# Optimization experiments

Measured on AMD Instinct MI355X. Metric: run time of the kernel, lower is better.

## Reference

```python
import jax, jax.numpy as jnp
import numpy as np

IN_DIM, HID, MID, FFN, OUT = 384, 128, 1024, 512, 1024
B, T = 8, 4096
LN_EPS = 1e-5


def _legs_hippo(n: int) -> np.ndarray:
    # A[i, j] = P_i(2j/n - 1) * sqrt(2i + 1), Legendre via 3-term recurrence
    x = 2.0 * np.arange(n) / n - 1.0          # eval points, shape [n]
    P = np.zeros((n, n), dtype=np.float64)     # P[i] = P_i(x)
    P[0] = 1.0
    if n > 1:
        P[1] = x
    for i in range(1, n - 1):
        P[i + 1] = ((2 * i + 1) * x * P[i] - i * P[i - 1]) / (i + 1)
    A = P * np.sqrt(2.0 * np.arange(n) + 1.0)[:, None]
    # rescale so the 4096-step recurrence stays finite (A is a free Parameter,
    # so any test value is valid; unscaled LegS overflows fp32 in ~20 steps)
    s = np.linalg.norm(A, 2)
    return (A / (1.05 * s)).astype(np.float32)


def _layernorm(x, g, b):
    mu = jnp.mean(x, axis=-1, keepdims=True)
    var = jnp.var(x, axis=-1, keepdims=True)
    return (x - mu) * jax.lax.rsqrt(var + LN_EPS) * g + b


def setup_inputs() -> dict:
    key = jax.random.key(0)
    ks = jax.random.split(key, 16)

    def w(k, shape, fan_in):
        return jax.random.normal(k, shape, jnp.float32) * (1.0 / np.sqrt(fan_in))

    return {
        "padded_x": jax.random.normal(ks[0], (B, T, IN_DIM), jnp.float32),
        "seq_lens": jax.random.randint(ks[1], (B,), 1, T + 1, jnp.int32),
        "A": jnp.asarray(_legs_hippo(HID)),
        "enc_w1": w(ks[2], (IN_DIM, MID), IN_DIM), "enc_b1": jnp.zeros((MID,), jnp.float32),
        "enc_w2": w(ks[3], (MID, HID), MID), "enc_b2": jnp.zeros((HID,), jnp.float32),
        "proj_w": w(ks[4], (HID, MID), HID), "proj_b": jnp.zeros((MID,), jnp.float32),
        "ln1_g": jnp.ones((MID,), jnp.float32), "ln1_b": jnp.zeros((MID,), jnp.float32),
        "ffn_w1": w(ks[5], (MID, FFN), MID), "ffn_b1": jnp.zeros((FFN,), jnp.float32),
        "ffn_w2": w(ks[6], (FFN, OUT), FFN), "ffn_b2": jnp.zeros((OUT,), jnp.float32),
        "ln2_g": jnp.ones((OUT,), jnp.float32), "ln2_b": jnp.zeros((OUT,), jnp.float32),
        "out_w": w(ks[7], (OUT, OUT), OUT), "out_b": jnp.zeros((OUT,), jnp.float32),
    }


def reference(padded_x, seq_lens, A, enc_w1, enc_b1, enc_w2, enc_b2,
              proj_w, proj_b, ln1_g, ln1_b, ffn_w1, ffn_b1, ffn_w2, ffn_b2,
              ln2_g, ln2_b, out_w, out_b):
    # encoder: Linear -> GELU(exact) -> Linear   [B, T, HID]
    h_mid = jax.nn.gelu(padded_x @ enc_w1 + enc_b1, approximate=False)
    seqs_bx = h_mid @ enc_w2 + enc_b2

    # masked linear recurrence h_t = A @ h_{t-1} + Bx_t via lax.scan over time
    xs = jnp.swapaxes(seqs_bx, 0, 1)           # [T, B, HID]
    ts = jnp.arange(xs.shape[0])

    def step(h, inp):
        x_t, t = inp
        upd = h @ A.T + x_t                     # (A @ h)^T batched
        mask = (t < seq_lens)[:, None]          # [B, 1]
        return jnp.where(mask, upd, h), None

    h0 = jnp.zeros((padded_x.shape[0], A.shape[0]), padded_x.dtype)
    batch_h, _ = jax.lax.scan(step, h0, (xs, ts))

    # decoder
    projected = batch_h @ proj_w + proj_b
    norm_h = _layernorm(projected, ln1_g, ln1_b)
    ffn_out = jax.nn.gelu(norm_h @ ffn_w1 + ffn_b1, approximate=False) @ ffn_w2 + ffn_b2
    ffn_out = ffn_out + projected               # residual (requires OUT == MID)
    norm_ffn = _layernorm(ffn_out, ln2_g, ln2_b)
    return norm_ffn @ out_w + out_b             # [B, OUT]
```

## Files before the change

### kernel.cpp

```cpp
#include <hip/hip_runtime.h>

typedef __attribute__((ext_vector_type(8))) short short8;
typedef __attribute__((ext_vector_type(4))) short short4v;
typedef __attribute__((ext_vector_type(4))) float float4v;

__device__ __forceinline__ float bf2f(short s) {
  union { float f; unsigned u; } cv; cv.u = ((unsigned)(unsigned short)s) << 16; return cv.f;
}
__device__ __forceinline__ short f2bf(float f) {
  union { float f; unsigned u; } cv; cv.f = f;
  unsigned u = cv.u;
  unsigned r = u + 0x7FFFu + ((u >> 16) & 1u);
  return (short)(r >> 16);
}
__device__ __forceinline__ float gelu_f(float v) {
  return 0.5f * v * (1.0f + erff(v * 0.70710678118654752440f));
}
__device__ __forceinline__ void glds16(const short* g, short* l) {
  __builtin_amdgcn_global_load_lds(
      (const __attribute__((address_space(1))) void*)g,
      (__attribute__((address_space(3))) void*)l, 16, 0, 0);
}

__global__ __launch_bounds__(256) void enc_fused(
    const short* __restrict__ xB, const short* __restrict__ w1T,
    const short* __restrict__ w2T, const float* __restrict__ b1,
    const float* __restrict__ b2, short* __restrict__ seqs,
    const int* __restrict__ seq_lens)
{
  int m0 = blockIdx.x * 64;
  { int b = m0 >> 12, t = m0 & 4095; if (t >= seq_lens[b]) return; }

  __shared__ __align__(16) short As[64 * 64];
  __shared__ __align__(16) short Ws[128 * 64];
  __shared__ __align__(16) short midb[64 * 128];

  int tid = threadIdx.x, lane = tid & 63, wave = tid >> 6;
  int l15 = lane & 15, quad = lane >> 4;
  int lr = lane >> 3, lseg = lane & 7;

  float4v accO[4][2];
#pragma unroll
  for (int i = 0; i < 4; i++)
#pragma unroll
    for (int j = 0; j < 2; j++) accO[i][j] = 0;

  for (int nc = 0; nc < 8; ++nc) {
    float4v accM[4][2];
#pragma unroll
    for (int i = 0; i < 4; i++)
#pragma unroll
      for (int j = 0; j < 2; j++) accM[i][j] = 0;

    for (int ks = 0; ks < 6; ++ks) {
      int kk = ks * 64;
#pragma unroll
      for (int i = 0; i < 2; i++) {
        int rowg = wave * 16 + i * 8;
        glds16(xB + (size_t)(m0 + rowg + lr) * 384 + kk + (lseg ^ lr) * 8, &As[rowg * 64]);
      }
#pragma unroll
      for (int i = 0; i < 4; i++) {
        int rowg = wave * 32 + i * 8;
        glds16(w1T + (size_t)(nc * 128 + rowg + lr) * 384 + kk + (lseg ^ lr) * 8, &Ws[rowg * 64]);
      }
      __syncthreads();
#pragma unroll
      for (int kh = 0; kh < 2; kh++) {
        int s = kh * 4 + quad;
        short8 af[4], bfr[2];
#pragma unroll
        for (int im = 0; im < 4; im++) {
          int r = im * 16 + l15;
          af[im] = *(short8*)&As[r * 64 + ((s ^ (r & 7)) * 8)];
        }
#pragma unroll
        for (int in = 0; in < 2; in++) {
          int r = wave * 32 + in * 16 + l15;
          bfr[in] = *(short8*)&Ws[r * 64 + ((s ^ (r & 7)) * 8)];
        }
#pragma unroll
        for (int im = 0; im < 4; im++)
#pragma unroll
          for (int in = 0; in < 2; in++)
            accM[im][in] = __builtin_amdgcn_mfma_f32_16x16x32_bf16(af[im], bfr[in], accM[im][in], 0, 0, 0);
      }
      __syncthreads();
    }
#pragma unroll
    for (int im = 0; im < 4; im++)
#pragma unroll
      for (int in = 0; in < 2; in++) {
        int k = wave * 32 + in * 16 + l15;
        float bias = b1[nc * 128 + k];
#pragma unroll
        for (int reg = 0; reg < 4; reg++) {
          int m = im * 16 + quad * 4 + reg;
          float v = gelu_f(accM[im][in][reg] + bias);
          int s = k >> 3;
          int sw = (s & 8) | ((s & 7) ^ (m & 7));
          midb[m * 128 + sw * 8 + (k & 7)] = f2bf(v);
        }
      }
    __syncthreads();
#pragma unroll
    for (int ks2 = 0; ks2 < 2; ++ks2) {
      int kk = nc * 128 + ks2 * 64;
#pragma unroll
      for (int i = 0; i < 4; i++) {
        int rowg = wave * 32 + i * 8;
        glds16(w2T + (size_t)(rowg + lr) * 1024 + kk + (lseg ^ lr) * 8, &Ws[rowg * 64]);
      }
      __syncthreads();
#pragma unroll
      for (int kh = 0; kh < 2; kh++) {
        short8 af[4], bfr[2];
#pragma unroll
        for (int im = 0; im < 4; im++) {
          int m = im * 16 + l15;
          int kb = ks2 * 64 + kh * 32 + quad * 8;
          int s = kb >> 3;
          int sw = (s & 8) | ((s & 7) ^ (m & 7));
          af[im] = *(short8*)&midb[m * 128 + sw * 8];
        }
#pragma unroll
        for (int in = 0; in < 2; in++) {
          int r = wave * 32 + in * 16 + l15;
          int s = kh * 4 + quad;
          bfr[in] = *(short8*)&Ws[r * 64 + ((s ^ (r & 7)) * 8)];
        }
#pragma unroll
        for (int im = 0; im < 4; im++)
#pragma unroll
          for (int in = 0; in < 2; in++)
            accO[im][in] = __builtin_amdgcn_mfma_f32_16x16x32_bf16(af[im], bfr[in], accO[im][in], 0, 0, 0);
      }
      __syncthreads();
    }
  }
#pragma unroll
  for (int im = 0; im < 4; im++)
#pragma unroll
    for (int in = 0; in < 2; in++) {
      int n = wave * 32 + in * 16 + l15;
      float bias = b2[n];
#pragma unroll
      for (int reg = 0; reg < 4; reg++) {
        int m = m0 + im * 16 + quad * 4 + reg;
        seqs[(size_t)m * 128 + n] = f2bf(accO[im][in][reg] + bias);
      }
    }
}

__global__ __launch_bounds__(256) void gemm_bt(
    const short* __restrict__ A_, const short* __restrict__ BT,
    float* __restrict__ out, int lda, int ldb, int ldc,
    int kSteps, int kChunk)
{
  int m0 = blockIdx.y * 128;
  int n0 = blockIdx.x * 128;
  int kBase = blockIdx.z * kChunk;

  __shared__ __align__(16) short As[128 * 64];
  __shared__ __align__(16) short Bs[128 * 64];

  int tid = threadIdx.x;
  int lane = tid & 63, wave = tid >> 6;
  int l15 = lane & 15, quad = lane >> 4;
  int wm = wave & 1, wn = wave >> 1;
  int lr = lane >> 3, lseg = lane & 7;

  float4v acc[4][4];
#pragma unroll
  for (int i = 0; i < 4; i++)
#pragma unroll
    for (int j = 0; j < 4; j++) acc[i][j] = 0;

  for (int ks = 0; ks < kSteps; ++ks) {
    int kk = kBase + ks * 64;
#pragma unroll
    for (int i = 0; i < 4; i++) {
      int rowg = wave * 32 + i * 8;
      glds16(A_ + (size_t)(m0 + rowg + lr) * lda + kk + (lseg ^ lr) * 8, &As[rowg * 64]);
      glds16(BT + (size_t)(n0 + rowg + lr) * ldb + kk + (lseg ^ lr) * 8, &Bs[rowg * 64]);
    }
    __syncthreads();
#pragma unroll
    for (int kh = 0; kh < 2; kh++) {
      int s = kh * 4 + quad;
      short8 af[4], bfr[4];
#pragma unroll
      for (int im = 0; im < 4; im++) {
        int r = wm * 64 + im * 16 + l15;
        af[im] = *(short8*)&As[r * 64 + ((s ^ (r & 7)) * 8)];
      }
#pragma unroll
      for (int in = 0; in < 4; in++) {
        int r = wn * 64 + in * 16 + l15;
        bfr[in] = *(short8*)&Bs[r * 64 + ((s ^ (r & 7)) * 8)];
      }
#pragma unroll
      for (int im = 0; im < 4; im++)
#pragma unroll
        for (int in = 0; in < 4; in++)
          acc[im][in] = __builtin_amdgcn_mfma_f32_16x16x32_bf16(af[im], bfr[in], acc[im][in], 0, 0, 0);
    }
    __syncthreads();
  }
  float* outz = out + (size_t)blockIdx.z * 65536;
#pragma unroll
  for (int im = 0; im < 4; im++)
#pragma unroll
    for (int in = 0; in < 4; in++) {
      int n = n0 + wn * 64 + in * 16 + l15;
#pragma unroll
      for (int reg = 0; reg < 4; reg++) {
        int m = m0 + wm * 64 + im * 16 + quad * 4 + reg;
        outz[(size_t)m * ldc + n] = acc[im][in][reg];
      }
    }
}

__global__ void prep_wide(const float* __restrict__ x, const float* __restrict__ w1,
                          const float* __restrict__ w2,
                          const float* __restrict__ proj_w, const float* __restrict__ ffn_w1,
                          const float* __restrict__ ffn_w2, const float* __restrict__ out_w,
                          const float* __restrict__ A,
                          short* __restrict__ xB,
                          short* __restrict__ w1T, short* __restrict__ w2T,
                          short* __restrict__ projB, short* __restrict__ ffn1B,
                          short* __restrict__ ffn2B, short* __restrict__ outB,
                          short* __restrict__ P1, short* __restrict__ P1t,
                          short* __restrict__ P2t,
                          short* __restrict__ Spow, short* __restrict__ SpowT)
{
  int idx = blockIdx.x * 256 + threadIdx.x;
  if (idx < 3145728) {
    float4v v = ((const float4v*)x)[idx];
    short4v o;
#pragma unroll
    for (int j = 0; j < 4; j++) o[j] = f2bf(v[j]);
    ((short4v*)xB)[idx] = o;
    return;
  }
  idx -= 3145728;
  if (idx < 393216) {
    int n = idx / 384, k = idx % 384;
    w1T[idx] = f2bf(w1[k * 1024 + n]);
    return;
  }
  idx -= 393216;
  if (idx < 131072) {
    int n = idx / 1024, k = idx % 1024;
    w2T[idx] = f2bf(w2[k * 128 + n]);
    return;
  }
  idx -= 131072;
  if (idx < 131072) { projB[idx] = f2bf(proj_w[idx]); return; }
  idx -= 131072;
  if (idx < 524288) { ffn1B[idx] = f2bf(ffn_w1[idx]); return; }
  idx -= 524288;
  if (idx < 524288) { ffn2B[idx] = f2bf(ffn_w2[idx]); return; }
  idx -= 524288;
  if (idx < 1048576) { outB[idx] = f2bf(out_w[idx]); return; }
  idx -= 1048576;
  if (idx < 16384) {
    int i = idx >> 7, j = idx & 127;
    short bidv = f2bf((i == j) ? 1.0f : 0.0f);
    P1[i * 8192 + 63 * 128 + j] = bidv;
    P1t[(63 * 128 + j) * 128 + i] = bidv;
    P2t[(63 * 128 + j) * 128 + i] = bidv;
    short ab = f2bf(A[idx]);
    Spow[idx] = ab;
    SpowT[(size_t)j * 128 + i] = ab;
  }
}

__global__ __launch_bounds__(256) void pow_chain(short* __restrict__ Spow,
                                                 short* __restrict__ SpowT)
{
  __shared__ short X[16384];
  __shared__ short XT[16384];
  int t = threadIdx.x;
  for (int i = t * 8; i < 16384; i += 2048) {
    *(short8*)&X[i]  = *(const short8*)&Spow[i];
    *(short8*)&XT[i] = *(const short8*)&SpowT[i];
  }
  __syncthreads();
  int lane = t & 63, wave = t >> 6, l15 = lane & 15, quad = lane >> 4;
  for (int step = 1; step <= 11; ++step) {
    short8 af[2][4], bfr[8][4];
#pragma unroll
    for (int mt = 0; mt < 2; mt++)
#pragma unroll
      for (int ks = 0; ks < 4; ks++)
        af[mt][ks] = *(short8*)&X[(wave * 32 + mt * 16 + l15) * 128 + ks * 32 + quad * 8];
#pragma unroll
    for (int nt = 0; nt < 8; nt++)
#pragma unroll
      for (int ks = 0; ks < 4; ks++)
        bfr[nt][ks] = *(short8*)&XT[(nt * 16 + l15) * 128 + ks * 32 + quad * 8];
    __syncthreads();
    float4v acc[2][8];
#pragma unroll
    for (int mt = 0; mt < 2; mt++)
#pragma unroll
      for (int nt = 0; nt < 8; nt++) acc[mt][nt] = 0;
#pragma unroll
    for (int ks = 0; ks < 4; ks++)
#pragma unroll
      for (int mt = 0; mt < 2; mt++)
#pragma unroll
        for (int nt = 0; nt < 8; nt++)
          acc[mt][nt] = __builtin_amdgcn_mfma_f32_16x16x32_bf16(af[mt][ks], bfr[nt][ks], acc[mt][nt], 0, 0, 0);
    short* gX  = Spow  + (size_t)step * 16384;
    short* gXT = SpowT + (size_t)step * 16384;
#pragma unroll
    for (int mt = 0; mt < 2; mt++)
#pragma unroll
      for (int nt = 0; nt < 8; nt++)
#pragma unroll
        for (int reg = 0; reg < 4; reg++) {
          int m = wave * 32 + mt * 16 + quad * 4 + reg;
          int n = nt * 16 + l15;
          short v = f2bf(acc[mt][nt][reg]);
          X[m * 128 + n] = v; XT[n * 128 + m] = v;
          gX[m * 128 + n] = v; gXT[n * 128 + m] = v;
        }
    __syncthreads();
  }
}

__global__ __launch_bounds__(256) void pow_fill(const short* __restrict__ Spow,
                                                const short* __restrict__ SpowT,
                                                short* __restrict__ P1,
                                                short* __restrict__ P1t,
                                                short* __restrict__ P2t)
{
  __shared__ short cur[16384];
  __shared__ short Bt[16384];
  int bid = blockIdx.x;
  int table1 = bid < 63;
  int e = table1 ? bid + 1 : bid - 62;
  int t = threadIdx.x;
  int lane = t & 63, wave = t >> 6, l15 = lane & 15, quad = lane >> 4;

  int bits = e;
  int k0 = __ffs(bits) - 1; bits &= bits - 1;
  int s0 = table1 ? k0 : (k0 == 0 ? 6 : 6 + k0);
  for (int i = t * 8; i < 16384; i += 2048)
    *(short8*)&cur[i] = *(const short8*)&Spow[(size_t)s0 * 16384 + i];

  while (bits) {
    int k = __ffs(bits) - 1; bits &= bits - 1;
    int si = table1 ? k : (k == 0 ? 6 : 6 + k);
    for (int i = t * 8; i < 16384; i += 2048)
      *(short8*)&Bt[i] = *(const short8*)&SpowT[(size_t)si * 16384 + i];
    __syncthreads();
    short8 af[2][4], bfr[8][4];
#pragma unroll
    for (int mt = 0; mt < 2; mt++)
#pragma unroll
      for (int ks = 0; ks < 4; ks++)
        af[mt][ks] = *(short8*)&cur[(wave * 32 + mt * 16 + l15) * 128 + ks * 32 + quad * 8];
#pragma unroll
    for (int nt = 0; nt < 8; nt++)
#pragma unroll
      for (int ks = 0; ks < 4; ks++)
        bfr[nt][ks] = *(short8*)&Bt[(nt * 16 + l15) * 128 + ks * 32 + quad * 8];
    __syncthreads();
    float4v acc[2][8];
#pragma unroll
    for (int mt = 0; mt < 2; mt++)
#pragma unroll
      for (int nt = 0; nt < 8; nt++) acc[mt][nt] = 0;
#pragma unroll
    for (int ks = 0; ks < 4; ks++)
#pragma unroll
      for (int mt = 0; mt < 2; mt++)
#pragma unroll
        for (int nt = 0; nt < 8; nt++)
          acc[mt][nt] = __builtin_amdgcn_mfma_f32_16x16x32_bf16(af[mt][ks], bfr[nt][ks], acc[mt][nt], 0, 0, 0);
#pragma unroll
    for (int mt = 0; mt < 2; mt++)
#pragma unroll
      for (int nt = 0; nt < 8; nt++)
#pragma unroll
        for (int reg = 0; reg < 4; reg++) {
          int m = wave * 32 + mt * 16 + quad * 4 + reg;
          int n = nt * 16 + l15;
          cur[m * 128 + n] = f2bf(acc[mt][nt][reg]);
        }
    __syncthreads();
  }
  __syncthreads();
  int slot = 63 - e;
  for (int idx = t; idx < 16384; idx += 256) {
    int i = idx >> 7, j = idx & 127;
    short v = cur[idx];
    if (table1) {
      P1[i * 8192 + slot * 128 + j] = v;
      P1t[(slot * 128 + j) * 128 + i] = v;
    } else {
      P2t[(slot * 128 + j) * 128 + i] = v;
    }
  }
}

__global__ __launch_bounds__(256) void combine_gemm(
    const float* __restrict__ Vz, const short* __restrict__ seqs,
    const int* __restrict__ seq_lens,
    const short* __restrict__ P2t, const short* __restrict__ P1t,
    float* __restrict__ hFtail)
{
  __shared__ short X[512 * 8];
  int pp = blockIdx.x >> 4, ks = blockIdx.x & 15;
  int t = threadIdx.x;
  for (int e = t; e < 4096; e += 256) {
    int klocal = e >> 3, b = e & 7;
    int cp = ks * 4 + (klocal >> 7), i = klocal & 127;
    int L = seq_lens[b];
    if (pp == 0) {
      int F = L >> 6, sh = 64 - F;
      float v = 0.f;
      if (cp >= sh) {
        int row = (b * 64 + (cp - sh)) * 128 + i;
#pragma unroll
        for (int z = 0; z < 16; z++) v += Vz[(size_t)z * 65536 + row];
      }
      X[e] = f2bf(v);
    } else {
      int F = L >> 6, rr = L & 63, sh = 64 - rr;
      short s = 0;
      if (cp >= sh) s = seqs[((size_t)b * 4096 + F * 64 + (cp - sh)) * 128 + i];
      X[e] = s;
    }
  }
  __syncthreads();
  const short* P = pp ? P1t : P2t;
  float* outp = hFtail + pp * 1024;
  int i = t & 127, g = t >> 7;
  float acc[4] = {0, 0, 0, 0};
  for (int kl = 0; kl < 512; ++kl) {
    int k = ks * 512 + kl;
    float pv = bf2f(P[k * 128 + i]);
    short4v xv = *(const short4v*)(X + kl * 8 + g * 4);
#pragma unroll
    for (int q = 0; q < 4; q++) acc[q] += bf2f(xv[q]) * pv;
  }
#pragma unroll
  for (int q = 0; q < 4; q++) atomicAdd(&outp[(g * 4 + q) * 128 + i], acc[q]);
}

__global__ __launch_bounds__(256) void proj_stage(
    const float* __restrict__ hFtail, const short* __restrict__ P1t,
    const int* __restrict__ seq_lens, const short* __restrict__ projB,
    const float* __restrict__ proj_b, float* __restrict__ projected)
{
  __shared__ short hT[128 * 8];
  __shared__ float red[4][64][8];
  int t = threadIdx.x;
  {
    int b = t >> 5, i4 = (t & 31) * 4;
    int rr = seq_lens[b] & 63;
    const short* M = P1t + (size_t)(63 - rr) * 128 * 128;
    const float* hF = hFtail + b * 128;
    float acc[4];
#pragma unroll
    for (int q = 0; q < 4; q++) acc[q] = hFtail[1024 + b * 128 + i4 + q];
    for (int j = 0; j < 128; ++j) {
      float hv = hF[j];
      short4v mv = *(const short4v*)&M[j * 128 + i4];
#pragma unroll
      for (int q = 0; q < 4; q++) acc[q] += bf2f(mv[q]) * hv;
    }
#pragma unroll
    for (int q = 0; q < 4; q++) hT[(i4 + q) * 8 + b] = f2bf(acc[q]);
  }
  __syncthreads();
  int c = t & 63, sl = t >> 6;
  int n = blockIdx.x * 64 + c;
  float acc[8] = {0, 0, 0, 0, 0, 0, 0, 0};
  for (int k = sl * 32; k < sl * 32 + 32; ++k) {
    short8 xv = *(short8*)&hT[k * 8];
    float wv = bf2f(projB[k * 1024 + n]);
#pragma unroll
    for (int b = 0; b < 8; b++) acc[b] += bf2f(xv[b]) * wv;
  }
#pragma unroll
  for (int b = 0; b < 8; b++) red[sl][c][b] = acc[b];
  __syncthreads();
  if (sl == 0) {
#pragma unroll
    for (int s = 1; s < 4; s++)
#pragma unroll
      for (int b = 0; b < 8; b++) acc[b] += red[s][c][b];
    float bn = proj_b[n];
#pragma unroll
    for (int b = 0; b < 8; b++) projected[b * 1024 + n] = acc[b] + bn;
  }
}

__global__ __launch_bounds__(256) void ffn1_stage(
    const float* __restrict__ projected, const float* __restrict__ g1,
    const float* __restrict__ b1, const short* __restrict__ ffn1B,
    float* __restrict__ ffn1raw)
{
  __shared__ float part[8][32][2];
  __shared__ float stats[8][2];
  __shared__ short xT[256 * 8];
  __shared__ float red[4][64][8];
  int t = threadIdx.x;
  { int b = t >> 5, j0 = t & 31; float s = 0, q = 0;
    for (int k = j0 * 32; k < j0 * 32 + 32; ++k) { float v = projected[b * 1024 + k]; s += v; q += v * v; }
    part[b][j0][0] = s; part[b][j0][1] = q; }
  __syncthreads();
  if (t < 8) {
    float s = 0, q = 0;
    for (int j = 0; j < 32; j++) { s += part[t][j][0]; q += part[t][j][1]; }
    float mu = s * (1.0f / 1024.0f);
    float var = q * (1.0f / 1024.0f) - mu * mu;
    stats[t][0] = mu; stats[t][1] = rsqrtf(var + 1e-5f);
  }
  __syncthreads();
  int ky0 = blockIdx.y * 256;
  for (int idx = t; idx < 2048; idx += 256) {
    int kl = idx >> 3, b = idx & 7; int k = ky0 + kl;
    float v = (projected[b * 1024 + k] - stats[b][0]) * stats[b][1] * g1[k] + b1[k];
    xT[kl * 8 + b] = f2bf(v);
  }
  __syncthreads();
  int c = t & 63, sl = t >> 6;
  int n = blockIdx.x * 64 + c;
  float acc[8] = {0, 0, 0, 0, 0, 0, 0, 0};
  for (int kl = sl * 64; kl < sl * 64 + 64; ++kl) {
    short8 xv = *(short8*)&xT[kl * 8];
    float wv = bf2f(ffn1B[(size_t)(ky0 + kl) * 512 + n]);
#pragma unroll
    for (int b = 0; b < 8; b++) acc[b] += bf2f(xv[b]) * wv;
  }
#pragma unroll
  for (int b = 0; b < 8; b++) red[sl][c][b] = acc[b];
  __syncthreads();
  if (sl == 0) {
#pragma unroll
    for (int s = 1; s < 4; s++)
#pragma unroll
      for (int b = 0; b < 8; b++) acc[b] += red[s][c][b];
#pragma unroll
    for (int b = 0; b < 8; b++) atomicAdd(&ffn1raw[b * 512 + n], acc[b]);
  }
}

__global__ __launch_bounds__(256) void ffn2_stage(
    const float* __restrict__ ffn1raw, const float* __restrict__ fb1,
    const short* __restrict__ ffn2B, float* __restrict__ ffn2raw)
{
  __shared__ short xT[256 * 8];
  __shared__ float red[4][64][8];
  int t = threadIdx.x;
  int ky0 = blockIdx.y * 256;
  for (int idx = t; idx < 2048; idx += 256) {
    int kl = idx >> 3, b = idx & 7; int k = ky0 + kl;
    float v = gelu_f(ffn1raw[b * 512 + k] + fb1[k]);
    xT[kl * 8 + b] = f2bf(v);
  }
  __syncthreads();
  int c = t & 63, sl = t >> 6;
  int n = blockIdx.x * 64 + c;
  float acc[8] = {0, 0, 0, 0, 0, 0, 0, 0};
  for (int kl = sl * 64; kl < sl * 64 + 64; ++kl) {
    short8 xv = *(short8*)&xT[kl * 8];
    float wv = bf2f(ffn2B[(size_t)(ky0 + kl) * 1024 + n]);
#pragma unroll
    for (int b = 0; b < 8; b++) acc[b] += bf2f(xv[b]) * wv;
  }
#pragma unroll
  for (int b = 0; b < 8; b++) red[sl][c][b] = acc[b];
  __syncthreads();
  if (sl == 0) {
#pragma unroll
    for (int s = 1; s < 4; s++)
#pragma unroll
      for (int b = 0; b < 8; b++) acc[b] += red[s][c][b];
#pragma unroll
    for (int b = 0; b < 8; b++) atomicAdd(&ffn2raw[b * 1024 + n], acc[b]);
  }
}

__global__ __launch_bounds__(256) void out_stage(
    const float* __restrict__ ffn2raw, const float* __restrict__ fb2,
    const float* __restrict__ projected, const float* __restrict__ g2,
    const float* __restrict__ b2ln, const short* __restrict__ outB,
    const float* __restrict__ out_b, float* __restrict__ d_out)
{
  __shared__ float part[8][32][2];
  __shared__ float stats[8][2];
  __shared__ short xT[512 * 8];
  __shared__ float red[4][64][8];
  int t = threadIdx.x;
  { int b = t >> 5, j0 = t & 31; float s = 0, q = 0;
    for (int k = j0 * 32; k < j0 * 32 + 32; ++k) {
      float v = ffn2raw[b * 1024 + k] + fb2[k] + projected[b * 1024 + k];
      s += v; q += v * v;
    }
    part[b][j0][0] = s; part[b][j0][1] = q; }
  __syncthreads();
  if (t < 8) {
    float s = 0, q = 0;
    for (int j = 0; j < 32; j++) { s += part[t][j][0]; q += part[t][j][1]; }
    float mu = s * (1.0f / 1024.0f);
    float var = q * (1.0f / 1024.0f) - mu * mu;
    stats[t][0] = mu; stats[t][1] = rsqrtf(var + 1e-5f);
  }
  __syncthreads();
  int ky0 = blockIdx.y * 512;
  for (int idx = t; idx < 4096; idx += 256) {
    int kl = idx >> 3, b = idx & 7; int k = ky0 + kl;
    float v = ffn2raw[b * 1024 + k] + fb2[k] + projected[b * 1024 + k];
    v = (v - stats[b][0]) * stats[b][1] * g2[k] + b2ln[k];
    xT[kl * 8 + b] = f2bf(v);
  }
  __syncthreads();
  int c = t & 63, sl = t >> 6;
  int n = blockIdx.x * 64 + c;
  float acc[8] = {0, 0, 0, 0, 0, 0, 0, 0};
  for (int kl = sl * 128; kl < sl * 128 + 128; ++kl) {
    short8 xv = *(short8*)&xT[kl * 8];
    float wv = bf2f(outB[(size_t)(ky0 + kl) * 1024 + n]);
#pragma unroll
    for (int b = 0; b < 8; b++) acc[b] += bf2f(xv[b]) * wv;
  }
#pragma unroll
  for (int b = 0; b < 8; b++) red[sl][c][b] = acc[b];
  __syncthreads();
  if (sl == 0) {
#pragma unroll
    for (int s = 1; s < 4; s++)
#pragma unroll
      for (int b = 0; b < 8; b++) acc[b] += red[s][c][b];
    float bn = (blockIdx.y == 0) ? out_b[n] : 0.0f;
#pragma unroll
    for (int b = 0; b < 8; b++) atomicAdd(&d_out[b * 1024 + n], acc[b] + bn);
  }
}

extern "C" void kernel_launch(void* const* d_in, const int* in_sizes, int n_in,
                              void* d_out, int out_size, void* d_ws, size_t ws_size,
                              hipStream_t stream)
{
  (void)in_sizes; (void)n_in; (void)out_size; (void)ws_size;
  const float* x      = (const float*)d_in[0];
  const int* seq_lens = (const int*)d_in[1];
  const float* A      = (const float*)d_in[2];
  const float* enc_w1 = (const float*)d_in[3];
  const float* enc_b1 = (const float*)d_in[4];
  const float* enc_w2 = (const float*)d_in[5];
  const float* enc_b2 = (const float*)d_in[6];
  const float* proj_w = (const float*)d_in[7];
  const float* proj_b = (const float*)d_in[8];
  const float* ln1_g  = (const float*)d_in[9];
  const float* ln1_b  = (const float*)d_in[10];
  const float* ffn_w1 = (const float*)d_in[11];
  const float* ffn_b1 = (const float*)d_in[12];
  const float* ffn_w2 = (const float*)d_in[13];
  const float* ffn_b2 = (const float*)d_in[14];
  const float* ln2_g  = (const float*)d_in[15];
  const float* ln2_b  = (const float*)d_in[16];
  const float* out_w  = (const float*)d_in[17];
  const float* out_b  = (const float*)d_in[18];

  char* p = (char*)d_ws;
  auto alloc = [&](size_t bytes) { char* r = p; p += (bytes + 255) & ~(size_t)255; return r; };
  short* xB    = (short*)alloc(32768ull * 384 * 2);
  short* seqs  = (short*)alloc(32768ull * 128 * 2);
  short* w1T   = (short*)alloc(1024ull * 384 * 2);
  short* w2T   = (short*)alloc(128ull * 1024 * 2);
  short* projB = (short*)alloc(128ull * 1024 * 2);
  short* ffn1B = (short*)alloc(1024ull * 512 * 2);
  short* ffn2B = (short*)alloc(512ull * 1024 * 2);
  short* outB  = (short*)alloc(1024ull * 1024 * 2);
  short* Spow  = (short*)alloc(12ull * 16384 * 2);
  short* SpowT = (short*)alloc(12ull * 16384 * 2);
  short* P1    = (short*)alloc(128ull * 8192 * 2);
  short* P1t   = (short*)alloc(8192ull * 128 * 2);
  short* P2t   = (short*)alloc(8192ull * 128 * 2);
  float* Vz    = (float*)alloc(16ull * 512 * 128 * 4);
  float* hFtail  = (float*)alloc(2ull * 8 * 128 * 4);
  float* ffn1raw = (float*)alloc(8ull * 512 * 4);
  float* ffn2raw = (float*)alloc(8ull * 1024 * 4);
  float* projected = (float*)alloc(8ull * 1024 * 4);

  hipMemsetAsync(hFtail, 0, (2ull * 8 * 128 + 8ull * 512 + 8ull * 1024) * 4, stream);
  hipMemsetAsync(d_out, 0, 8192ull * 4, stream);

  prep_wide<<<23104, 256, 0, stream>>>(x, enc_w1, enc_w2, proj_w, ffn_w1, ffn_w2, out_w, A,
      xB, w1T, w2T, projB, ffn1B, ffn2B, outB, P1, P1t, P2t, Spow, SpowT);
  pow_chain<<<1, 256, 0, stream>>>(Spow, SpowT);
  pow_fill<<<126, 256, 0, stream>>>(Spow, SpowT, P1, P1t, P2t);

  enc_fused<<<512, 256, 0, stream>>>(xB, w1T, w2T, enc_b1, enc_b2, seqs, seq_lens);

  gemm_bt<<<dim3(1, 4, 16), 256, 0, stream>>>(seqs, P1, Vz, 8192, 8192, 128, 8, 512);
  combine_gemm<<<32, 256, 0, stream>>>(Vz, seqs, seq_lens, P2t, P1t, hFtail);

  proj_stage<<<16, 256, 0, stream>>>(hFtail, P1t, seq_lens, projB, proj_b, projected);
  ffn1_stage<<<dim3(8, 4), 256, 0, stream>>>(projected, ln1_g, ln1_b, ffn1B, ffn1raw);
  ffn2_stage<<<dim3(16, 2), 256, 0, stream>>>(ffn1raw, ffn_b1, ffn2B, ffn2raw);
  out_stage<<<dim3(16, 2), 256, 0, stream>>>(ffn2raw, ffn_b2, projected, ln2_g, ln2_b,
      outB, out_b, (float*)d_out);
}
```

Before: 428.9 us.

## Split encoder over MID chunks, skip padded x conversion, deepen split-K

The fused encoder now splits its MID dimension across four blocks in a second grid axis. Each block writes fp32 partial sums, and a new reduce kernel adds the four partials plus bias and converts to bf16, so about four times as many blocks can keep the device busy. The x-to-bf16 conversion now skips rows past each sequence's length. The split-K for the gemm_bt/combine_gemm stage doubles from 16 to 32 chunks. The cost is extra fp32 partial traffic (a 64MB workspace), one more kernel launch, and a longer sum over Vz slices in combine.

```diff
diff --git a/kernel.cpp b/kernel.cpp
--- a/kernel.cpp
+++ b/kernel.cpp
@@ -25,11 +25,11 @@
 __global__ __launch_bounds__(256) void enc_fused(
     const short* __restrict__ xB, const short* __restrict__ w1T,
     const short* __restrict__ w2T, const float* __restrict__ b1,
-    const float* __restrict__ b2, short* __restrict__ seqs,
-    const int* __restrict__ seq_lens)
+    float* __restrict__ encP, const int* __restrict__ seq_lens)
 {
   int m0 = blockIdx.x * 64;
   { int b = m0 >> 12, t = m0 & 4095; if (t >= seq_lens[b]) return; }
+  int nc0 = blockIdx.y * 2;
 
   __shared__ __align__(16) short As[64 * 64];
   __shared__ __align__(16) short Ws[128 * 64];
@@ -45,7 +45,8 @@
 #pragma unroll
     for (int j = 0; j < 2; j++) accO[i][j] = 0;
 
-  for (int nc = 0; nc < 8; ++nc) {
+  for (int nci = 0; nci < 2; ++nci) {
+    int nc = nc0 + nci;
     float4v accM[4][2];
 #pragma unroll
     for (int i = 0; i < 4; i++)
@@ -138,18 +139,46 @@
       __syncthreads();
     }
   }
+  float* outp = encP + ((size_t)blockIdx.y << 22);
 #pragma unroll
   for (int im = 0; im < 4; im++)
 #pragma unroll
     for (int in = 0; in < 2; in++) {
       int n = wave * 32 + in * 16 + l15;
-      float bias = b2[n];
 #pragma unroll
       for (int reg = 0; reg < 4; reg++) {
         int m = m0 + im * 16 + quad * 4 + reg;
-        seqs[(size_t)m * 128 + n] = f2bf(accO[im][in][reg] + bias);
-      }
-    }
+        outp[(size_t)m * 128 + n] = accO[im][in][reg];
+      }
+    }
+}
+
+__global__ __launch_bounds__(256) void enc_reduce(
+    const float* __restrict__ encP, const float* __restrict__ b2,
+    short* __restrict__ seqs, const int* __restrict__ seq_lens)
+{
+  int m0 = blockIdx.x * 64;
+  { int b = m0 >> 12, t = m0 & 4095; if (t >= seq_lens[b]) return; }
+  int t = threadIdx.x;
+#pragma unroll
+  for (int i = 0; i < 8; i++) {
+    int f4 = t + i * 256;
+    int m = m0 + (f4 >> 5);
+    int cg = f4 & 31;
+    size_t off = (size_t)m * 128 + cg * 4;
+    float4v v = *(const float4v*)&encP[off];
+#pragma unroll
+    for (int y = 1; y < 4; y++) {
+      float4v w = *(const float4v*)&encP[((size_t)y << 22) + off];
+#pragma unroll
+      for (int q = 0; q < 4; q++) v[q] += w[q];
+    }
+    float4v bb = *(const float4v*)&b2[cg * 4];
+    short4v o;
+#pragma unroll
+    for (int q = 0; q < 4; q++) o[q] = f2bf(v[q] + bb[q]);
+    *(short4v*)&seqs[off] = o;
+  }
 }
 
 __global__ __launch_bounds__(256) void gemm_bt(
@@ -225,7 +254,7 @@
                           const float* __restrict__ w2,
                           const float* __restrict__ proj_w, const float* __restrict__ ffn_w1,
                           const float* __restrict__ ffn_w2, const float* __restrict__ out_w,
-                          const float* __restrict__ A,
+                          const float* __restrict__ A, const int* __restrict__ seq_lens,
                           short* __restrict__ xB,
                           short* __restrict__ w1T, short* __restrict__ w2T,
                           short* __restrict__ projB, short* __restrict__ ffn1B,
@@ -236,6 +265,9 @@
 {
   int idx = blockIdx.x * 256 + threadIdx.x;
   if (idx < 3145728) {
+    int row = idx / 96;
+    int t = row & 4095, b = row >> 12;
+    if (t >= seq_lens[b]) return;
     float4v v = ((const float4v*)x)[idx];
     short4v o;
 #pragma unroll
@@ -413,12 +445,12 @@
     const short* __restrict__ P2t, const short* __restrict__ P1t,
     float* __restrict__ hFtail)
 {
-  __shared__ short X[512 * 8];
-  int pp = blockIdx.x >> 4, ks = blockIdx.x & 15;
+  __shared__ short X[256 * 8];
+  int pp = blockIdx.x >> 5, ks = blockIdx.x & 31;
   int t = threadIdx.x;
-  for (int e = t; e < 4096; e += 256) {
+  for (int e = t; e < 2048; e += 256) {
     int klocal = e >> 3, b = e & 7;
-    int cp = ks * 4 + (klocal >> 7), i = klocal & 127;
+    int cp = ks * 2 + (klocal >> 7), i = klocal & 127;
     int L = seq_lens[b];
     if (pp == 0) {
       int F = L >> 6, sh = 64 - F;
@@ -426,7 +458,7 @@
       if (cp >= sh) {
         int row = (b * 64 + (cp - sh)) * 128 + i;
 #pragma unroll
-        for (int z = 0; z < 16; z++) v += Vz[(size_t)z * 65536 + row];
+        for (int z = 0; z < 32; z++) v += Vz[(size_t)z * 65536 + row];
       }
       X[e] = f2bf(v);
     } else {
@@ -441,8 +473,8 @@
   float* outp = hFtail + pp * 1024;
   int i = t & 127, g = t >> 7;
   float acc[4] = {0, 0, 0, 0};
-  for (int kl = 0; kl < 512; ++kl) {
-    int k = ks * 512 + kl;
+  for (int kl = 0; kl < 256; ++kl) {
+    int k = ks * 256 + kl;
     float pv = bf2f(P[k * 128 + i]);
     short4v xv = *(const short4v*)(X + kl * 8 + g * 4);
 #pragma unroll
@@ -673,6 +705,7 @@
   char* p = (char*)d_ws;
   auto alloc = [&](size_t bytes) { char* r = p; p += (bytes + 255) & ~(size_t)255; return r; };
   short* xB    = (short*)alloc(32768ull * 384 * 2);
+  float* encP  = (float*)alloc(4ull * 32768 * 128 * 4);
   short* seqs  = (short*)alloc(32768ull * 128 * 2);
   short* w1T   = (short*)alloc(1024ull * 384 * 2);
   short* w2T   = (short*)alloc(128ull * 1024 * 2);
@@ -685,7 +718,7 @@
   short* P1    = (short*)alloc(128ull * 8192 * 2);
   short* P1t   = (short*)alloc(8192ull * 128 * 2);
   short* P2t   = (short*)alloc(8192ull * 128 * 2);
-  float* Vz    = (float*)alloc(16ull * 512 * 128 * 4);
+  float* Vz    = (float*)alloc(32ull * 512 * 128 * 4);
   float* hFtail  = (float*)alloc(2ull * 8 * 128 * 4);
   float* ffn1raw = (float*)alloc(8ull * 512 * 4);
   float* ffn2raw = (float*)alloc(8ull * 1024 * 4);
@@ -695,14 +728,15 @@
   hipMemsetAsync(d_out, 0, 8192ull * 4, stream);
 
   prep_wide<<<23104, 256, 0, stream>>>(x, enc_w1, enc_w2, proj_w, ffn_w1, ffn_w2, out_w, A,
-      xB, w1T, w2T, projB, ffn1B, ffn2B, outB, P1, P1t, P2t, Spow, SpowT);
+      seq_lens, xB, w1T, w2T, projB, ffn1B, ffn2B, outB, P1, P1t, P2t, Spow, SpowT);
   pow_chain<<<1, 256, 0, stream>>>(Spow, SpowT);
   pow_fill<<<126, 256, 0, stream>>>(Spow, SpowT, P1, P1t, P2t);
 
-  enc_fused<<<512, 256, 0, stream>>>(xB, w1T, w2T, enc_b1, enc_b2, seqs, seq_lens);
-
-  gemm_bt<<<dim3(1, 4, 16), 256, 0, stream>>>(seqs, P1, Vz, 8192, 8192, 128, 8, 512);
-  combine_gemm<<<32, 256, 0, stream>>>(Vz, seqs, seq_lens, P2t, P1t, hFtail);
+  enc_fused<<<dim3(512, 4), 256, 0, stream>>>(xB, w1T, w2T, enc_b1, encP, seq_lens);
+  enc_reduce<<<512, 256, 0, stream>>>(encP, enc_b2, seqs, seq_lens);
+
+  gemm_bt<<<dim3(1, 4, 32), 256, 0, stream>>>(seqs, P1, Vz, 8192, 8192, 128, 4, 256);
+  combine_gemm<<<64, 256, 0, stream>>>(Vz, seqs, seq_lens, P2t, P1t, hFtail);
 
   proj_stage<<<16, 256, 0, stream>>>(hFtail, P1t, seq_lens, projB, proj_b, projected);
   ffn1_stage<<<dim3(8, 4), 256, 0, stream>>>(projected, ln1_g, ln1_b, ffn1B, ffn1raw);
```

Result: faster. 405.4 us (-5.5%).
